# Performance work log

Hardware: AMD Instinct MI355X
Metric: run time of the kernel (lower is better)

The kernel has to match this reference:

```python
import jax, jax.numpy as jnp
import numpy as np

EPS = 1e-5
NEG = 0.1  # LeakyReLU slope


def _conv(x, w, stride=1, pad=0):
    return jax.lax.conv_general_dilated(
        x, w, (stride, stride), [(pad, pad), (pad, pad)],
        dimension_numbers=('NCHW', 'OIHW', 'NCHW'))


def _bn(x, p):
    # p: [4, C] stacked (gamma, beta, running_mean, running_var); eval-mode BN
    g, b, m, v = p[0], p[1], p[2], p[3]
    inv = g / jnp.sqrt(v + EPS)
    return x * inv[None, :, None, None] + (b - m * inv)[None, :, None, None]


def _lrelu(x):
    return jnp.where(x >= 0, x, NEG * x)


def _mdcn(x, w_off, b_off, w_dcn, b_dcn, G=2, K=3, pad=1):
    # ModulatedDeformConvPack (DCNv2): conv_offset -> (dy, dx, mask), then
    # modulated bilinear sampling + dense contraction with the conv weight.
    B, C, H, W = x.shape
    K2 = K * K
    off = _conv(x, w_off, 1, pad) + b_off[None, :, None, None]  # [B, 3*G*K2, H, W]
    dy, dx, ml = jnp.split(off, 3, axis=1)
    dy = dy.reshape(B, G, K2, H, W)
    dx = dx.reshape(B, G, K2, H, W)
    mask = jax.nn.sigmoid(ml).reshape(B, G, K2, H, W)
    kyv, kxv = np.meshgrid(np.arange(K), np.arange(K), indexing='ij')
    ky = jnp.asarray(kyv.reshape(K2), x.dtype)
    kx = jnp.asarray(kxv.reshape(K2), x.dtype)
    ii = jnp.arange(H, dtype=x.dtype)
    jj = jnp.arange(W, dtype=x.dtype)
    # sample coords: p0 + p_k + offset (stride 1, dilation 1)
    py = ii[None, None, None, :, None] - pad + ky[None, None, :, None, None] + dy
    px = jj[None, None, None, None, :] - pad + kx[None, None, :, None, None] + dx
    Cg = C // G
    # [B, G, H*W, Cg] layout so the bilinear gather indexes a small int tensor
    imgs = x.reshape(B, G, Cg, H, W).transpose(0, 1, 3, 4, 2).reshape(B, G, H * W, Cg)
    y0 = jnp.floor(py)
    x0 = jnp.floor(px)
    N = K2 * H * W
    wy = (py - y0).reshape(B, G, N, 1)
    wx = (px - x0).reshape(B, G, N, 1)

    def gather(yi, xi):
        valid = (yi >= 0) & (yi <= H - 1) & (xi >= 0) & (xi <= W - 1)
        yc = jnp.clip(yi, 0, H - 1).astype(jnp.int32)
        xc = jnp.clip(xi, 0, W - 1).astype(jnp.int32)
        idx = (yc * W + xc).reshape(B, G, N, 1)
        v = jnp.take_along_axis(imgs, idx, axis=2)  # [B, G, N, Cg]
        return v * valid.reshape(B, G, N, 1).astype(x.dtype)

    v00 = gather(y0, x0)
    v01 = gather(y0, x0 + 1)
    v10 = gather(y0 + 1, x0)
    v11 = gather(y0 + 1, x0 + 1)
    val = (v00 * (1 - wy) * (1 - wx) + v01 * (1 - wy) * wx
           + v10 * wy * (1 - wx) + v11 * wy * wx)
    val = (val * mask.reshape(B, G, N, 1)).reshape(B, G, K2, H, W, Cg)
    wr = w_dcn.reshape(w_dcn.shape[0], G, Cg, K2)
    out = jnp.einsum('bgkijc,ogck->boij', val, wr)
    return out + b_dcn[None, :, None, None]


def _forward(x, w_r1, bn_r1, w_r2, bn_r2, w_rs, bn_rs, w_off, b_off,
             w_dcn, b_dcn, bn1, w_c2, bn2, w_ds, bn_ds):
    # ResBlock(in=64, out=128, stride=2): conv3x3/s2-BN-LReLU-conv3x3-BN + 1x1/s2 shortcut
    h = _lrelu(_bn(_conv(x, w_r1, 2, 1), bn_r1))
    h = _bn(_conv(h, w_r2, 1, 1), bn_r2)
    sc = _bn(_conv(x, w_rs, 2, 0), bn_rs)
    h = _lrelu(h + sc)
    # modulated deformable conv 3x3, deformable_groups=2
    h = _lrelu(_bn(_mdcn(h, w_off, b_off, w_dcn, b_dcn), bn1))
    h = _lrelu(_bn(_conv(h, w_c2, 1, 0), bn2))
    # DeconBlock residual (downsample since in!=out, stride!=1)
    res = _bn(_conv(x, w_ds, 2, 0), bn_ds)
    return res + h


def setup_inputs() -> dict:
    key = jax.random.key(0)
    ks = jax.random.split(key, 16)
    f32 = jnp.float32

    def n(k, shape, s):
        return jax.random.normal(k, shape, f32) * s

    def bnp(k, c):
        # gamma, beta, mean, var — var kept >= 0.1 for stability
        return jax.random.uniform(k, (4, c), f32, 0.1, 1.0)

    return {
        'x': n(ks[0], (4, 64, 192, 192), 1.0),
        'w_r1': n(ks[1], (128, 64, 3, 3), 0.04),
        'bn_r1': bnp(ks[2], 128),
        'w_r2': n(ks[3], (128, 128, 3, 3), 0.03),
        'bn_r2': bnp(ks[4], 128),
        'w_rs': n(ks[5], (128, 64, 1, 1), 0.12),
        'bn_rs': bnp(ks[6], 128),
        'w_off': n(ks[7], (54, 128, 3, 3), 0.01),  # small => offsets of a few px
        'b_off': n(ks[8], (54,), 0.1),
        'w_dcn': n(ks[9], (128, 128, 3, 3), 0.03),
        'b_dcn': n(ks[10], (128,), 0.1),
        'bn1': bnp(ks[11], 128),
        'w_c2': n(ks[12], (128, 128, 1, 1), 0.09),
        'bn2': bnp(ks[13], 128),
        'w_ds': n(ks[14], (128, 64, 1, 1), 0.12),
        'bn_ds': bnp(ks[15], 128),
    }


def reference(x, w_r1, bn_r1, w_r2, bn_r2, w_rs, bn_rs, w_off, b_off,
              w_dcn, b_dcn, bn1, w_c2, bn2, w_ds, bn_ds):
    return _forward(x, w_r1, bn_r1, w_r2, bn_r2, w_rs, bn_rs, w_off, b_off,
                    w_dcn, b_dcn, bn1, w_c2, bn2, w_ds, bn_ds)
```

## Files before the change

kernel.cpp:

```cpp
#include <hip/hip_runtime.h>
#include <hip/hip_bf16.h>
#include <cstdint>

#define EPS 1e-5f
#define NEG 0.1f

using bfrag = __attribute__((ext_vector_type(8))) short;
using f32x4 = __attribute__((ext_vector_type(4))) float;
typedef unsigned short ushort_t;

constexpr int B_  = 4,  CIN = 64, H0 = 192, W0 = 192;
constexpr int C_  = 128, H_ = 96, W_ = 96;
constexpr int HW_ = H_ * W_;
constexpr int HW0 = H0 * W0;
constexpr int XS  = 194;
constexpr int TS  = 98;
constexpr int VSTR = 1160;

__device__ __forceinline__ ushort_t f2bf(float f) {
  unsigned u = __builtin_bit_cast(unsigned, f);
  u += 0x7fffu + ((u >> 16) & 1u);
  return (ushort_t)(u >> 16);
}
__device__ __forceinline__ float loF(unsigned d) {
  return __builtin_bit_cast(float, d << 16);
}
__device__ __forceinline__ float hiF(unsigned d) {
  return __builtin_bit_cast(float, d & 0xFFFF0000u);
}
__device__ __forceinline__ bfrag loadB(const ushort_t* p) {
  return *(const bfrag*)p;
}

#define MFMA4(A0, A1, B0, B1, ACC)                                             \
  ACC[0][0] = __builtin_amdgcn_mfma_f32_16x16x32_bf16(A0, B0, ACC[0][0], 0, 0, 0); \
  ACC[0][1] = __builtin_amdgcn_mfma_f32_16x16x32_bf16(A0, B1, ACC[0][1], 0, 0, 0); \
  ACC[1][0] = __builtin_amdgcn_mfma_f32_16x16x32_bf16(A1, B0, ACC[1][0], 0, 0, 0); \
  ACC[1][1] = __builtin_amdgcn_mfma_f32_16x16x32_bf16(A1, B1, ACC[1][1], 0, 0, 0);

__global__ __launch_bounds__(256)
void k_prep(const float* __restrict__ w_r1, const float* __restrict__ w_r2,
            const float* __restrict__ w_off, const float* __restrict__ w_dcn,
            const float* __restrict__ w_rs, const float* __restrict__ w_c2,
            const float* __restrict__ w_ds,
            ushort_t* __restrict__ wp_r1, ushort_t* __restrict__ wp_r2,
            ushort_t* __restrict__ wp_off, ushort_t* __restrict__ wp_dcn,
            ushort_t* __restrict__ wp_rs, ushort_t* __restrict__ wp_c2,
            ushort_t* __restrict__ wp_ds,
            ushort_t* __restrict__ xclp, ushort_t* __restrict__ t1p,
            ushort_t* __restrict__ t3p) {
  int bi = blockIdx.x;
  int tid = (int)threadIdx.x;
  auto pack3w = [&](const float* w, ushort_t* wp, int O, int C, int Opad, int b0) {
    int idx = (bi - b0) * 256 + tid;
    int e = idx & 7;
    int lane = (idx >> 3) & 63;
    int fb = idx >> 9;
    int OBQ = Opad / 16;
    int obq = fb % OBQ, s = fb / OBQ;
    int lr = lane & 15, lq = lane >> 4;
    int o = obq * 16 + lr;
    int cq = s % (C / 32), tap = s / (C / 32);
    int c = cq * 32 + lq * 8 + e;
    wp[idx] = (o < O) ? f2bf(w[((size_t)o * C + c) * 9 + tap]) : (ushort_t)0;
  };
  auto pack1w = [&](const float* w, ushort_t* wp, int O, int C, int Opad, int b0) {
    int idx = (bi - b0) * 256 + tid;
    int e = idx & 7;
    int lane = (idx >> 3) & 63;
    int fb = idx >> 9;
    int OBQ = Opad / 16;
    int obq = fb % OBQ, s = fb / OBQ;
    int lr = lane & 15, lq = lane >> 4;
    int o = obq * 16 + lr;
    int c = s * 32 + lq * 8 + e;
    wp[idx] = (o < O) ? f2bf(w[(size_t)o * C + c]) : (ushort_t)0;
  };
  auto border = [&](ushort_t* buf, int N, int C, int b0) {
    int idx = (bi - b0) * 256 + tid;
    int per = 4 * N - 4;
    if (idx >= per * 4) return;
    int b = idx / per, e = idx - b * per;
    int r, s;
    if (e < N) { r = 0; s = e; }
    else if (e < 2 * N) { r = N - 1; s = e - N; }
    else if (e < 3 * N - 2) { r = e - 2 * N + 1; s = 0; }
    else { r = e - (3 * N - 2) + 1; s = N - 1; }
    uint4* p = (uint4*)(buf + ((size_t)(b * N + r) * N + s) * C);
#pragma unroll
    for (int t = 0; t < 16; ++t) { if (t < C / 8) p[t] = make_uint4(0, 0, 0, 0); }
  };
  if      (bi <  288) pack3w(w_r1,  wp_r1, 128,  64, 128, 0);
  else if (bi <  864) pack3w(w_r2,  wp_r2, 128, 128, 128, 288);
  else if (bi < 1152) pack3w(w_off, wp_off, 54, 128,  64, 864);
  else if (bi < 1728) pack3w(w_dcn, wp_dcn, 128, 128, 128, 1152);
  else if (bi < 1760) pack1w(w_rs,  wp_rs, 128,  64, 128, 1728);
  else if (bi < 1824) pack1w(w_c2,  wp_c2, 128, 128, 128, 1760);
  else if (bi < 1856) pack1w(w_ds,  wp_ds, 128,  64, 128, 1824);
  else if (bi < 1869) border(xclp, XS, 64, 1856);
  else if (bi < 1876) border(t1p, TS, 128, 1869);
  else                border(t3p, TS, 128, 1876);
}

__global__ __launch_bounds__(256)
void k_xcl(const float* __restrict__ x, ushort_t* __restrict__ xclp) {
  __shared__ float tile[64][65];
  int tx = threadIdx.x, ty = threadIdx.y;
  int cx = blockIdx.x, y = blockIdx.y, b = blockIdx.z;
  const float* src = x + (size_t)b * CIN * HW0 + (size_t)y * W0 + cx * 64;
#pragma unroll
  for (int r = 0; r < 16; ++r) {
    int ch = r * 4 + ty;
    tile[ch][tx] = src[(size_t)ch * HW0 + tx];
  }
  __syncthreads();
  ushort_t* dst = xclp + ((size_t)(b * XS + y + 1) * XS + cx * 64 + 1) * 64;
#pragma unroll
  for (int r = 0; r < 16; ++r) {
    int pp = r * 4 + ty;
    dst[(size_t)pp * 64 + tx] = f2bf(tile[tx][pp]);
  }
}

__global__ __launch_bounds__(256)
void k_conv1(const ushort_t* __restrict__ xclp, const ushort_t* __restrict__ wp,
             const float* __restrict__ bnp, ushort_t* __restrict__ t1p) {
  __shared__ ushort_t at[5 * 66 * 64];
  int tid = threadIdx.x, lane = tid & 63, wv = tid >> 6;
  int lr = lane & 15, lq = lane >> 4, ob = wv * 32;
  int j0 = blockIdx.x * 32, i0 = blockIdx.y * 2, b = blockIdx.z;
  for (int t = tid; t < 2640; t += 256) {
    int ky = t / 528, r = t - ky * 528;
    int p = r >> 3, c8 = r & 7;
    const char* src = (const char*)(xclp +
        ((size_t)(b * XS + 2 * i0 + ky) * XS + 2 * j0) * 64) + p * 128 + c8 * 16;
    int db = ((ky * 66 + p) * 128 + c8 * 16) ^ (((p >> 1) & 7) << 4);
    *(uint4*)((char*)at + db) = *(const uint4*)src;
  }
  __syncthreads();
  f32x4 acc[2][2][2] = {};
#pragma unroll
  for (int tap = 0; tap < 9; ++tap) {
    int ky = tap / 3, kx = tap - 3 * ky;
    int pxa = 2 * lr + kx, pxb = 2 * (16 + lr) + kx;
#pragma unroll
    for (int cq = 0; cq < 2; ++cq) {
      int s = tap * 2 + cq;
      bfrag b0 = loadB(wp + (size_t)(s * 8 + wv * 2) * 512 + lane * 8);
      bfrag b1 = loadB(wp + (size_t)(s * 8 + wv * 2 + 1) * 512 + lane * 8);
#pragma unroll
      for (int r = 0; r < 2; ++r) {
        int kr = 2 * r + ky;
        bfrag a0 = *(const bfrag*)((const char*)at +
            (((kr * 66 + pxa) * 128 + cq * 64 + lq * 16) ^ (((pxa >> 1) & 7) << 4)));
        bfrag a1 = *(const bfrag*)((const char*)at +
            (((kr * 66 + pxb) * 128 + cq * 64 + lq * 16) ^ (((pxb >> 1) & 7) << 4)));
        MFMA4(a0, a1, b0, b1, acc[r]);
      }
    }
  }
#pragma unroll
  for (int r = 0; r < 2; ++r) {
    ushort_t* dst = t1p + ((size_t)(b * TS + i0 + r + 1) * TS + j0 + 1) * 128;
#pragma unroll
    for (int nf = 0; nf < 2; ++nf) {
      int o = ob + nf * 16 + lr;
      float inv = bnp[o] * rsqrtf(bnp[384 + o] + EPS);
      float bb = bnp[128 + o] - bnp[256 + o] * inv;
#pragma unroll
      for (int mf = 0; mf < 2; ++mf)
#pragma unroll
        for (int jj = 0; jj < 4; ++jj) {
          int pix = mf * 16 + 4 * lq + jj;
          float v = acc[r][mf][nf][jj] * inv + bb;
          v = v >= 0.f ? v : NEG * v;
          dst[(size_t)pix * 128 + o] = f2bf(v);
        }
    }
  }
}

__global__ __launch_bounds__(256)
void k_conv2(const ushort_t* __restrict__ t1p, const ushort_t* __restrict__ xclp,
             const ushort_t* __restrict__ wp2, const ushort_t* __restrict__ wprs,
             const float* __restrict__ bn2p, const float* __restrict__ bnsp,
             ushort_t* __restrict__ t3p) {
  __shared__ ushort_t at[4 * 34 * 128];
  int tid = threadIdx.x, lane = tid & 63, wv = tid >> 6;
  int lr = lane & 15, lq = lane >> 4, ob = wv * 32;
  int j0 = blockIdx.x * 32, i0 = blockIdx.y * 2, b = blockIdx.z;
  for (int t = tid; t < 2176; t += 256) {
    int ky = t / 544, r = t - ky * 544;
    int p = r >> 4, c16 = r & 15;
    const char* src = (const char*)(t1p +
        ((size_t)(b * TS + i0 + ky) * TS + j0) * 128) + p * 256 + c16 * 16;
    int db = ((ky * 34 + p) * 256 + c16 * 16) ^ ((p & 7) << 4);
    *(uint4*)((char*)at + db) = *(const uint4*)src;
  }
  __syncthreads();
  f32x4 acc[2][2][2] = {};
  f32x4 acs[2][2][2] = {};
#pragma unroll
  for (int tap = 0; tap < 9; ++tap) {
    int ky = tap / 3, kx = tap - 3 * ky;
    int pxa = lr + kx, pxb = 16 + lr + kx;
#pragma unroll
    for (int cq = 0; cq < 4; ++cq) {
      int s = tap * 4 + cq;
      bfrag b0 = loadB(wp2 + (size_t)(s * 8 + wv * 2) * 512 + lane * 8);
      bfrag b1 = loadB(wp2 + (size_t)(s * 8 + wv * 2 + 1) * 512 + lane * 8);
#pragma unroll
      for (int r = 0; r < 2; ++r) {
        int kr = r + ky;
        bfrag a0 = *(const bfrag*)((const char*)at +
            (((kr * 34 + pxa) * 256 + cq * 64 + lq * 16) ^ ((pxa & 7) << 4)));
        bfrag a1 = *(const bfrag*)((const char*)at +
            (((kr * 34 + pxb) * 256 + cq * 64 + lq * 16) ^ ((pxb & 7) << 4)));
        MFMA4(a0, a1, b0, b1, acc[r]);
      }
    }
  }
#pragma unroll
  for (int r = 0; r < 2; ++r) {
    const ushort_t* rowp = xclp + (size_t)(b * XS + 2 * (i0 + r) + 1) * XS * 64;
    const ushort_t* pa = rowp + (size_t)(2 * (j0 + lr) + 1) * 64 + 8 * lq;
    const ushort_t* pb = rowp + (size_t)(2 * (j0 + 16 + lr) + 1) * 64 + 8 * lq;
#pragma unroll
    for (int sq = 0; sq < 2; ++sq) {
      bfrag a0 = loadB(pa + sq * 32);
      bfrag a1 = loadB(pb + sq * 32);
      bfrag b0 = loadB(wprs + (size_t)(sq * 8 + wv * 2) * 512 + lane * 8);
      bfrag b1 = loadB(wprs + (size_t)(sq * 8 + wv * 2 + 1) * 512 + lane * 8);
      MFMA4(a0, a1, b0, b1, acs[r]);
    }
  }
#pragma unroll
  for (int r = 0; r < 2; ++r) {
    ushort_t* dst = t3p + ((size_t)(b * TS + i0 + r + 1) * TS + j0 + 1) * 128;
#pragma unroll
    for (int nf = 0; nf < 2; ++nf) {
      int o = ob + nf * 16 + lr;
      float i2 = bn2p[o] * rsqrtf(bn2p[384 + o] + EPS);
      float b2 = bn2p[128 + o] - bn2p[256 + o] * i2;
      float is = bnsp[o] * rsqrtf(bnsp[384 + o] + EPS);
      float bs = bnsp[128 + o] - bnsp[256 + o] * is;
#pragma unroll
      for (int mf = 0; mf < 2; ++mf)
#pragma unroll
        for (int jj = 0; jj < 4; ++jj) {
          int pix = mf * 16 + 4 * lq + jj;
          float h = acc[r][mf][nf][jj] * i2 + b2 + acs[r][mf][nf][jj] * is + bs;
          h = h >= 0.f ? h : NEG * h;
          dst[(size_t)pix * 128 + o] = f2bf(h);
        }
    }
  }
}

__global__ __launch_bounds__(128)
void k_convoff(const ushort_t* __restrict__ t3p, const ushort_t* __restrict__ wp,
               const float* __restrict__ boff, float* __restrict__ offb) {
  __shared__ ushort_t at[3 * 34 * 128];
  int tid = threadIdx.x, lane = tid & 63, wv = tid >> 6;
  int lr = lane & 15, lq = lane >> 4, ob = wv * 32;
  int j0 = blockIdx.x * 32, i = blockIdx.y, b = blockIdx.z;
  for (int t = tid; t < 1632; t += 128) {
    int ky = t / 544, r = t - ky * 544;
    int p = r >> 4, c16 = r & 15;
    const char* src = (const char*)(t3p +
        ((size_t)(b * TS + i + ky) * TS + j0) * 128) + p * 256 + c16 * 16;
    int db = ((ky * 34 + p) * 256 + c16 * 16) ^ ((p & 7) << 4);
    *(uint4*)((char*)at + db) = *(const uint4*)src;
  }
  __syncthreads();
  f32x4 acc[2][2] = {};
#pragma unroll
  for (int tap = 0; tap < 9; ++tap) {
    int ky = tap / 3, kx = tap - 3 * ky;
    int pxa = lr + kx, pxb = 16 + lr + kx;
#pragma unroll
    for (int cq = 0; cq < 4; ++cq) {
      bfrag a0 = *(const bfrag*)((const char*)at +
          (((ky * 34 + pxa) * 256 + cq * 64 + lq * 16) ^ ((pxa & 7) << 4)));
      bfrag a1 = *(const bfrag*)((const char*)at +
          (((ky * 34 + pxb) * 256 + cq * 64 + lq * 16) ^ ((pxb & 7) << 4)));
      int s = tap * 4 + cq;
      bfrag b0 = loadB(wp + (size_t)(s * 4 + wv * 2) * 512 + lane * 8);
      bfrag b1 = loadB(wp + (size_t)(s * 4 + wv * 2 + 1) * 512 + lane * 8);
      MFMA4(a0, a1, b0, b1, acc);
    }
  }
  float* dst = offb + ((size_t)b * HW_ + (size_t)i * W_ + j0) * 64;
#pragma unroll
  for (int nf = 0; nf < 2; ++nf) {
    int o = ob + nf * 16 + lr;
    float bias = (o < 54) ? boff[o] : 0.f;
#pragma unroll
    for (int mf = 0; mf < 2; ++mf)
#pragma unroll
      for (int jj = 0; jj < 4; ++jj) {
        int pix = mf * 16 + 4 * lq + jj;
        float v = (o < 54) ? acc[mf][nf][jj] + bias : 0.f;
        dst[(size_t)pix * 64 + o] = v;
      }
  }
}

__global__ __launch_bounds__(512)
void k_dcn(const ushort_t* __restrict__ t3p, const float* __restrict__ offb,
           const ushort_t* __restrict__ wp, const float* __restrict__ bdcn,
           const float* __restrict__ bnp, ushort_t* __restrict__ t4cl) {
  __shared__ ushort_t val[32 * VSTR];
  int tid = threadIdx.x;
  int j0 = blockIdx.x * 32, i = blockIdx.y, b = blockIdx.z;
  int lane = tid & 63, wv = tid >> 6;
  int gq = tid >> 4;
  int c16 = tid & 15;
  int gl = (gq & 3) * 16;

  int my_b0 = 0, my_b1 = 0;
  unsigned my_w00 = 0, my_w10 = 0, my_w01 = 0, my_w11 = 0;
  if (c16 < 9) {
    int k = c16;
    int ky = k / 3, kx = k - 3 * ky;
    int j = j0 + gq;
    const float* ob_ = offb + ((size_t)b * HW_ + (size_t)i * W_ + j) * 64;
#pragma unroll
    for (int g = 0; g < 2; ++g) {
      int gk = g * 9 + k;
      float dy = ob_[gk];
      float dx = ob_[18 + gk];
      float ml = ob_[36 + gk];
      float mk = 1.f / (1.f + __expf(-ml));
      float py = (float)(i - 1 + ky) + dy;
      float px = (float)(j - 1 + kx) + dx;
      float fy = floorf(py), fx = floorf(px);
      float wy = py - fy, wx = px - fx;
      int y0 = (int)fy, x0 = (int)fx;
      bool yv0 = (unsigned)y0 < 96u, yv1 = (unsigned)(y0 + 1) < 96u;
      bool xv0 = (unsigned)x0 < 96u, xv1 = (unsigned)(x0 + 1) < 96u;
      float w00 = (yv0 && xv0) ? (1.f - wy) * (1.f - wx) * mk : 0.f;
      float w01 = (yv0 && xv1) ? (1.f - wy) * wx * mk : 0.f;
      float w10 = (yv1 && xv0) ? wy * (1.f - wx) * mk : 0.f;
      float w11 = (yv1 && xv1) ? wy * wx * mk : 0.f;
      int yb = min(max(y0, -1), 95), xb = min(max(x0, -1), 95);
      int bb = (((yb + 1) * TS + xb + 1) * 128 + g * 64) * 2;
      unsigned pw0 = (unsigned)f2bf(w00) | ((unsigned)f2bf(w01) << 16);
      unsigned pw1 = (unsigned)f2bf(w10) | ((unsigned)f2bf(w11) << 16);
      if (g == 0) { my_b0 = bb; my_w00 = pw0; my_w10 = pw1; }
      else        { my_b1 = bb; my_w01 = pw0; my_w11 = pw1; }
    }
  }

  const char* imgb = (const char*)(t3p + (size_t)b * TS * TS * 128) + c16 * 8;
  char* vrow = (char*)val + gq * (VSTR * 2) + c16 * 8;

#pragma unroll
  for (int g = 0; g < 2; ++g) {
#pragma unroll
    for (int k = 0; k < 9; ++k) {
      int gb = __shfl(g == 0 ? my_b0 : my_b1, gl + k, 64);
      unsigned w0 = (unsigned)__shfl((int)(g == 0 ? my_w00 : my_w01), gl + k, 64);
      unsigned w1 = (unsigned)__shfl((int)(g == 0 ? my_w10 : my_w11), gl + k, 64);
      const char* pA = imgb + gb;
      uint2 d00 = *(const uint2*)pA;
      uint2 d01 = *(const uint2*)(pA + 256);
      uint2 d10 = *(const uint2*)(pA + TS * 256);
      uint2 d11 = *(const uint2*)(pA + TS * 256 + 256);
      float w00 = loF(w0), w01 = hiF(w0);
      float w10 = loF(w1), w11 = hiF(w1);
      unsigned o2[2];
#pragma unroll
      for (int t = 0; t < 2; ++t) {
        unsigned e00 = ((const unsigned*)&d00)[t];
        unsigned e01 = ((const unsigned*)&d01)[t];
        unsigned e10 = ((const unsigned*)&d10)[t];
        unsigned e11 = ((const unsigned*)&d11)[t];
        float slo = loF(e00) * w00 + loF(e01) * w01 + loF(e10) * w10 + loF(e11) * w11;
        float shi = hiF(e00) * w00 + hiF(e01) * w01 + hiF(e10) * w10 + hiF(e11) * w11;
        unsigned u0 = __builtin_bit_cast(unsigned, slo) + 0x8000u;
        unsigned u1 = __builtin_bit_cast(unsigned, shi) + 0x8000u;
        o2[t] = __builtin_amdgcn_perm(u1, u0, 0x07060302u);
      }
      *(uint2*)(vrow + k * 256 + g * 128) = make_uint2(o2[0], o2[1]);
    }
  }
  __syncthreads();

  int lr = lane & 15, lq = lane >> 4, ob = wv * 16;
  f32x4 acc0 = {}, acc1 = {};
  for (int s = 0; s < 36; ++s) {
    bfrag a0 = *(const bfrag*)&val[lr * VSTR + 32 * s + 8 * lq];
    bfrag a1 = *(const bfrag*)&val[(16 + lr) * VSTR + 32 * s + 8 * lq];
    bfrag b0 = loadB(wp + (size_t)(s * 8 + wv) * 512 + lane * 8);
    acc0 = __builtin_amdgcn_mfma_f32_16x16x32_bf16(a0, b0, acc0, 0, 0, 0);
    acc1 = __builtin_amdgcn_mfma_f32_16x16x32_bf16(a1, b0, acc1, 0, 0, 0);
  }

  {
    ushort_t* dst = t4cl + ((size_t)(b * 96 + i) * 96 + j0) * 128;
    int o = ob + lr;
    float inv = bnp[o] * rsqrtf(bnp[384 + o] + EPS);
    float bb = bnp[128 + o] - bnp[256 + o] * inv;
    float bd = bdcn[o];
#pragma unroll
    for (int jj = 0; jj < 4; ++jj) {
      int p0 = 4 * lq + jj;
      float r0 = (acc0[jj] + bd) * inv + bb;
      r0 = r0 >= 0.f ? r0 : NEG * r0;
      dst[(size_t)p0 * 128 + o] = f2bf(r0);
      float r1 = (acc1[jj] + bd) * inv + bb;
      r1 = r1 >= 0.f ? r1 : NEG * r1;
      dst[(size_t)(16 + p0) * 128 + o] = f2bf(r1);
    }
  }
}

__global__ __launch_bounds__(256)
void k_final(const ushort_t* __restrict__ t4cl, const ushort_t* __restrict__ xclp,
             const ushort_t* __restrict__ wpc2, const ushort_t* __restrict__ wpds,
             const float* __restrict__ bn2p, const float* __restrict__ bndsp,
             float* __restrict__ outp) {
  __shared__ float ol[128 * 36];
  int tid = threadIdx.x, lane = tid & 63, wv = tid >> 6;
  int lr = lane & 15, lq = lane >> 4, ob = wv * 32;
  int j0 = blockIdx.x * 32, i = blockIdx.y, b = blockIdx.z;
  f32x4 acc[2][2] = {};
  f32x4 acs[2][2] = {};
  {
    const ushort_t* rowp = t4cl + ((size_t)(b * 96 + i) * 96 + j0) * 128;
#pragma unroll
    for (int s = 0; s < 4; ++s) {
      bfrag a0 = loadB(rowp + (size_t)lr * 128 + s * 32 + 8 * lq);
      bfrag a1 = loadB(rowp + (size_t)(16 + lr) * 128 + s * 32 + 8 * lq);
      bfrag b0 = loadB(wpc2 + (size_t)(s * 8 + wv * 2) * 512 + lane * 8);
      bfrag b1 = loadB(wpc2 + (size_t)(s * 8 + wv * 2 + 1) * 512 + lane * 8);
      MFMA4(a0, a1, b0, b1, acc);
    }
  }
  {
    const ushort_t* rowx = xclp + (size_t)(b * XS + 2 * i + 1) * XS * 64;
    const ushort_t* pa = rowx + (size_t)(2 * (j0 + lr) + 1) * 64 + 8 * lq;
    const ushort_t* pb = rowx + (size_t)(2 * (j0 + 16 + lr) + 1) * 64 + 8 * lq;
#pragma unroll
    for (int s = 0; s < 2; ++s) {
      bfrag a0 = loadB(pa + s * 32);
      bfrag a1 = loadB(pb + s * 32);
      bfrag b0 = loadB(wpds + (size_t)(s * 8 + wv * 2) * 512 + lane * 8);
      bfrag b1 = loadB(wpds + (size_t)(s * 8 + wv * 2 + 1) * 512 + lane * 8);
      MFMA4(a0, a1, b0, b1, acs);
    }
  }
#pragma unroll
  for (int nf = 0; nf < 2; ++nf) {
    int o = ob + nf * 16 + lr;
    float i2 = bn2p[o] * rsqrtf(bn2p[384 + o] + EPS);
    float b2 = bn2p[128 + o] - bn2p[256 + o] * i2;
    float id = bndsp[o] * rsqrtf(bndsp[384 + o] + EPS);
    float bd = bndsp[128 + o] - bndsp[256 + o] * id;
#pragma unroll
    for (int mf = 0; mf < 2; ++mf)
#pragma unroll
      for (int jj = 0; jj < 4; ++jj) {
        int pix = mf * 16 + 4 * lq + jj;
        float h = acc[mf][nf][jj] * i2 + b2;
        h = h >= 0.f ? h : NEG * h;
        float res = acs[mf][nf][jj] * id + bd;
        ol[o * 36 + pix] = res + h;
      }
  }
  __syncthreads();
#pragma unroll
  for (int r = 0; r < 4; ++r) {
    int idx = r * 256 + tid;
    int o = idx >> 3, p4 = idx & 7;
    f32x4 v = *(const f32x4*)&ol[o * 36 + p4 * 4];
    *(f32x4*)&outp[((size_t)(b * C_ + o) * H_ + i) * W_ + j0 + p4 * 4] = v;
  }
}

extern "C" void kernel_launch(void* const* d_in, const int* in_sizes, int n_in,
                              void* d_out, int out_size, void* d_ws, size_t ws_size,
                              hipStream_t stream) {
  const float* x     = (const float*)d_in[0];
  const float* w_r1  = (const float*)d_in[1];
  const float* bn_r1 = (const float*)d_in[2];
  const float* w_r2  = (const float*)d_in[3];
  const float* bn_r2 = (const float*)d_in[4];
  const float* w_rs  = (const float*)d_in[5];
  const float* bn_rs = (const float*)d_in[6];
  const float* w_off = (const float*)d_in[7];
  const float* b_off = (const float*)d_in[8];
  const float* w_dcn = (const float*)d_in[9];
  const float* b_dcn = (const float*)d_in[10];
  const float* bn1   = (const float*)d_in[11];
  const float* w_c2  = (const float*)d_in[12];
  const float* bn2   = (const float*)d_in[13];
  const float* w_ds  = (const float*)d_in[14];
  const float* bn_ds = (const float*)d_in[15];
  float* out = (float*)d_out;

  ushort_t* base  = (ushort_t*)d_ws;
  ushort_t* xclp  = base;
  ushort_t* t1p   = base + 9634816;
  ushort_t* t3p   = base + 14552064;
  ushort_t* wp_r1 = base + 19469312;
  ushort_t* wp_r2 = wp_r1 + 73728;
  ushort_t* wp_off= wp_r2 + 147456;
  ushort_t* wp_dcn= wp_off + 73728;
  ushort_t* wp_rs = wp_dcn + 147456;
  ushort_t* wp_c2 = wp_rs + 8192;
  ushort_t* wp_ds = wp_c2 + 16384;
  float*    offb  = (float*)t1p;
  ushort_t* t4cl  = t1p;

  k_prep<<<1883, 256, 0, stream>>>(w_r1, w_r2, w_off, w_dcn, w_rs, w_c2, w_ds,
                                   wp_r1, wp_r2, wp_off, wp_dcn, wp_rs, wp_c2,
                                   wp_ds, xclp, t1p, t3p);

  k_xcl    <<<dim3(3, 192, 4), dim3(64, 4), 0, stream>>>(x, xclp);
  k_conv1  <<<dim3(3, 48, 4), 256, 0, stream>>>(xclp, wp_r1, bn_r1, t1p);
  k_conv2  <<<dim3(3, 48, 4), 256, 0, stream>>>(t1p, xclp, wp_r2, wp_rs, bn_r2, bn_rs, t3p);
  k_convoff<<<dim3(3, 96, 4), 128, 0, stream>>>(t3p, wp_off, b_off, offb);
  k_dcn    <<<dim3(3, 96, 4), 512, 0, stream>>>(t3p, offb, wp_dcn, b_dcn, bn1, t4cl);
  k_final  <<<dim3(3, 96, 4), 256, 0, stream>>>(t4cl, xclp, wp_c2, wp_ds, bn2, bn_ds, out);
}
```

Before: 128.1 us.

## Fuse offset conv into DCN kernel and merge input transpose into prep

The separate offset-convolution kernel is folded into the deformable-conv kernel. Each block now covers 16 pixels instead of 32, computes the 54 offset channels with MFMA (K split across two wave halves and reduced through LDS), and keeps the offsets in LDS instead of writing them to global memory. The NCHW-to-channel-last bf16 transpose of x is also moved into k_prep as extra blocks, which removes one more launch. The cost is a smaller per-block pixel tile, so each block does less work and reloads DCN weights more often.

Result: no change. 127.0 us (-0.9%).

```diff
diff --git a/kernel.cpp b/kernel.cpp
--- a/kernel.cpp
+++ b/kernel.cpp
@@ -39,7 +39,8 @@
   ACC[1][1] = __builtin_amdgcn_mfma_f32_16x16x32_bf16(A1, B1, ACC[1][1], 0, 0, 0);
 
 __global__ __launch_bounds__(256)
-void k_prep(const float* __restrict__ w_r1, const float* __restrict__ w_r2,
+void k_prep(const float* __restrict__ x,
+            const float* __restrict__ w_r1, const float* __restrict__ w_r2,
             const float* __restrict__ w_off, const float* __restrict__ w_dcn,
             const float* __restrict__ w_rs, const float* __restrict__ w_c2,
             const float* __restrict__ w_ds,
@@ -49,6 +50,7 @@
             ushort_t* __restrict__ wp_ds,
             ushort_t* __restrict__ xclp, ushort_t* __restrict__ t1p,
             ushort_t* __restrict__ t3p) {
+  __shared__ float tile[64][65];
   int bi = blockIdx.x;
   int tid = (int)threadIdx.x;
   auto pack3w = [&](const float* w, ushort_t* wp, int O, int C, int Opad, int b0) {
@@ -99,26 +101,26 @@
   else if (bi < 1856) pack1w(w_ds,  wp_ds, 128,  64, 128, 1824);
   else if (bi < 1869) border(xclp, XS, 64, 1856);
   else if (bi < 1876) border(t1p, TS, 128, 1869);
-  else                border(t3p, TS, 128, 1876);
-}
-
-__global__ __launch_bounds__(256)
-void k_xcl(const float* __restrict__ x, ushort_t* __restrict__ xclp) {
-  __shared__ float tile[64][65];
-  int tx = threadIdx.x, ty = threadIdx.y;
-  int cx = blockIdx.x, y = blockIdx.y, b = blockIdx.z;
-  const float* src = x + (size_t)b * CIN * HW0 + (size_t)y * W0 + cx * 64;
-#pragma unroll
-  for (int r = 0; r < 16; ++r) {
-    int ch = r * 4 + ty;
-    tile[ch][tx] = src[(size_t)ch * HW0 + tx];
-  }
-  __syncthreads();
-  ushort_t* dst = xclp + ((size_t)(b * XS + y + 1) * XS + cx * 64 + 1) * 64;
-#pragma unroll
-  for (int r = 0; r < 16; ++r) {
-    int pp = r * 4 + ty;
-    dst[(size_t)pp * 64 + tx] = f2bf(tile[tx][pp]);
+  else if (bi < 1883) border(t3p, TS, 128, 1876);
+  else {
+    int bx = bi - 1883;
+    int cx = bx % 3;
+    int rem = bx / 3;
+    int y = rem % 192, b = rem / 192;
+    int tx = tid & 63, ty = tid >> 6;
+    const float* src = x + (size_t)b * CIN * HW0 + (size_t)y * W0 + cx * 64;
+#pragma unroll
+    for (int r = 0; r < 16; ++r) {
+      int ch = r * 4 + ty;
+      tile[ch][tx] = src[(size_t)ch * HW0 + tx];
+    }
+    __syncthreads();
+    ushort_t* dst = xclp + ((size_t)(b * XS + y + 1) * XS + cx * 64 + 1) * 64;
+#pragma unroll
+    for (int r = 0; r < 16; ++r) {
+      int pp = r * 4 + ty;
+      dst[(size_t)pp * 64 + tx] = f2bf(tile[tx][pp]);
+    }
   }
 }
 
@@ -257,144 +259,130 @@
   }
 }
 
-__global__ __launch_bounds__(128)
-void k_convoff(const ushort_t* __restrict__ t3p, const ushort_t* __restrict__ wp,
-               const float* __restrict__ boff, float* __restrict__ offb) {
-  __shared__ ushort_t at[3 * 34 * 128];
-  int tid = threadIdx.x, lane = tid & 63, wv = tid >> 6;
-  int lr = lane & 15, lq = lane >> 4, ob = wv * 32;
-  int j0 = blockIdx.x * 32, i = blockIdx.y, b = blockIdx.z;
-  for (int t = tid; t < 1632; t += 128) {
-    int ky = t / 544, r = t - ky * 544;
-    int p = r >> 4, c16 = r & 15;
-    const char* src = (const char*)(t3p +
-        ((size_t)(b * TS + i + ky) * TS + j0) * 128) + p * 256 + c16 * 16;
-    int db = ((ky * 34 + p) * 256 + c16 * 16) ^ ((p & 7) << 4);
-    *(uint4*)((char*)at + db) = *(const uint4*)src;
-  }
-  __syncthreads();
-  f32x4 acc[2][2] = {};
-#pragma unroll
-  for (int tap = 0; tap < 9; ++tap) {
-    int ky = tap / 3, kx = tap - 3 * ky;
-    int pxa = lr + kx, pxb = 16 + lr + kx;
-#pragma unroll
-    for (int cq = 0; cq < 4; ++cq) {
-      bfrag a0 = *(const bfrag*)((const char*)at +
-          (((ky * 34 + pxa) * 256 + cq * 64 + lq * 16) ^ ((pxa & 7) << 4)));
-      bfrag a1 = *(const bfrag*)((const char*)at +
-          (((ky * 34 + pxb) * 256 + cq * 64 + lq * 16) ^ ((pxb & 7) << 4)));
-      int s = tap * 4 + cq;
-      bfrag b0 = loadB(wp + (size_t)(s * 4 + wv * 2) * 512 + lane * 8);
-      bfrag b1 = loadB(wp + (size_t)(s * 4 + wv * 2 + 1) * 512 + lane * 8);
-      MFMA4(a0, a1, b0, b1, acc);
-    }
-  }
-  float* dst = offb + ((size_t)b * HW_ + (size_t)i * W_ + j0) * 64;
-#pragma unroll
-  for (int nf = 0; nf < 2; ++nf) {
-    int o = ob + nf * 16 + lr;
-    float bias = (o < 54) ? boff[o] : 0.f;
-#pragma unroll
-    for (int mf = 0; mf < 2; ++mf)
+__global__ __launch_bounds__(512)
+void k_dcn(const ushort_t* __restrict__ t3p, const ushort_t* __restrict__ wpo,
+           const float* __restrict__ boff, const ushort_t* __restrict__ wp,
+           const float* __restrict__ bdcn, const float* __restrict__ bnp,
+           ushort_t* __restrict__ t4cl) {
+  __shared__ ushort_t val[16 * VSTR];
+  __shared__ float offb_lds[16 * 64];
+  int tid = threadIdx.x;
+  int j0 = blockIdx.x * 16, i = blockIdx.y, b = blockIdx.z;
+  int lane = tid & 63, wv = tid >> 6;
+  int lr = lane & 15, lq = lane >> 4;
+
+  {
+    char* at = (char*)val;
+    for (int t = tid; t < 864; t += 512) {
+      int ky = t / 288, r = t - ky * 288;
+      int p = r >> 4, c16b = r & 15;
+      const char* src = (const char*)(t3p +
+          ((size_t)(b * TS + i + ky) * TS + j0 + p) * 128) + c16b * 16;
+      int db = ((ky * 18 + p) * 256 + c16b * 16) ^ ((p & 7) << 4);
+      *(uint4*)(at + db) = *(const uint4*)src;
+    }
+    __syncthreads();
+    int ot = wv & 3, kh = wv >> 2;
+    f32x4 pacc = {};
+#pragma unroll
+    for (int s9 = 0; s9 < 18; ++s9) {
+      int s = kh * 18 + s9;
+      int tap = s >> 2, cq = s & 3;
+      int ky = tap / 3, kx = tap - 3 * ky;
+      int px = lr + kx;
+      bfrag a0 = *(const bfrag*)(at +
+          (((ky * 18 + px) * 256 + cq * 64 + lq * 16) ^ ((px & 7) << 4)));
+      bfrag b0 = loadB(wpo + (size_t)(s * 4 + ot) * 512 + lane * 8);
+      pacc = __builtin_amdgcn_mfma_f32_16x16x32_bf16(a0, b0, pacc, 0, 0, 0);
+    }
+    float* red = (float*)((char*)val + 16384);
+    if (kh == 1) {
+      *(f32x4*)(red + ot * 256 + lane * 4) = pacc;
+    }
+    __syncthreads();
+    if (kh == 0) {
+      f32x4 v = *(const f32x4*)(red + ot * 256 + lane * 4);
+      pacc += v;
+      int o = ot * 16 + lr;
+      float bias = (o < 54) ? boff[o] : 0.f;
 #pragma unroll
       for (int jj = 0; jj < 4; ++jj) {
-        int pix = mf * 16 + 4 * lq + jj;
-        float v = (o < 54) ? acc[mf][nf][jj] + bias : 0.f;
-        dst[(size_t)pix * 64 + o] = v;
+        int px = 4 * lq + jj;
+        offb_lds[px * 64 + o] = pacc[jj] + bias;
       }
-  }
-}
-
-__global__ __launch_bounds__(512)
-void k_dcn(const ushort_t* __restrict__ t3p, const float* __restrict__ offb,
-           const ushort_t* __restrict__ wp, const float* __restrict__ bdcn,
-           const float* __restrict__ bnp, ushort_t* __restrict__ t4cl) {
-  __shared__ ushort_t val[32 * VSTR];
-  int tid = threadIdx.x;
-  int j0 = blockIdx.x * 32, i = blockIdx.y, b = blockIdx.z;
-  int lane = tid & 63, wv = tid >> 6;
+    }
+    __syncthreads();
+  }
+
   int gq = tid >> 4;
   int c16 = tid & 15;
+  int pix = gq >> 1, g = gq & 1;
   int gl = (gq & 3) * 16;
-
-  int my_b0 = 0, my_b1 = 0;
-  unsigned my_w00 = 0, my_w10 = 0, my_w01 = 0, my_w11 = 0;
+  int my_b = 0; unsigned my_w0 = 0, my_w1 = 0;
   if (c16 < 9) {
-    int k = c16;
+    int k = c16, gk = g * 9 + k;
     int ky = k / 3, kx = k - 3 * ky;
-    int j = j0 + gq;
-    const float* ob_ = offb + ((size_t)b * HW_ + (size_t)i * W_ + j) * 64;
-#pragma unroll
-    for (int g = 0; g < 2; ++g) {
-      int gk = g * 9 + k;
-      float dy = ob_[gk];
-      float dx = ob_[18 + gk];
-      float ml = ob_[36 + gk];
-      float mk = 1.f / (1.f + __expf(-ml));
-      float py = (float)(i - 1 + ky) + dy;
-      float px = (float)(j - 1 + kx) + dx;
-      float fy = floorf(py), fx = floorf(px);
-      float wy = py - fy, wx = px - fx;
-      int y0 = (int)fy, x0 = (int)fx;
-      bool yv0 = (unsigned)y0 < 96u, yv1 = (unsigned)(y0 + 1) < 96u;
-      bool xv0 = (unsigned)x0 < 96u, xv1 = (unsigned)(x0 + 1) < 96u;
-      float w00 = (yv0 && xv0) ? (1.f - wy) * (1.f - wx) * mk : 0.f;
-      float w01 = (yv0 && xv1) ? (1.f - wy) * wx * mk : 0.f;
-      float w10 = (yv1 && xv0) ? wy * (1.f - wx) * mk : 0.f;
-      float w11 = (yv1 && xv1) ? wy * wx * mk : 0.f;
-      int yb = min(max(y0, -1), 95), xb = min(max(x0, -1), 95);
-      int bb = (((yb + 1) * TS + xb + 1) * 128 + g * 64) * 2;
-      unsigned pw0 = (unsigned)f2bf(w00) | ((unsigned)f2bf(w01) << 16);
-      unsigned pw1 = (unsigned)f2bf(w10) | ((unsigned)f2bf(w11) << 16);
-      if (g == 0) { my_b0 = bb; my_w00 = pw0; my_w10 = pw1; }
-      else        { my_b1 = bb; my_w01 = pw0; my_w11 = pw1; }
-    }
-  }
+    int j = j0 + pix;
+    const float* ob_ = offb_lds + pix * 64;
+    float dy = ob_[gk];
+    float dx = ob_[18 + gk];
+    float ml = ob_[36 + gk];
+    float mk = 1.f / (1.f + __expf(-ml));
+    float py = (float)(i - 1 + ky) + dy;
+    float px = (float)(j - 1 + kx) + dx;
+    float fy = floorf(py), fx = floorf(px);
+    float wy = py - fy, wx = px - fx;
+    int y0 = (int)fy, x0 = (int)fx;
+    bool yv0 = (unsigned)y0 < 96u, yv1 = (unsigned)(y0 + 1) < 96u;
+    bool xv0 = (unsigned)x0 < 96u, xv1 = (unsigned)(x0 + 1) < 96u;
+    float w00 = (yv0 && xv0) ? (1.f - wy) * (1.f - wx) * mk : 0.f;
+    float w01 = (yv0 && xv1) ? (1.f - wy) * wx * mk : 0.f;
+    float w10 = (yv1 && xv0) ? wy * (1.f - wx) * mk : 0.f;
+    float w11 = (yv1 && xv1) ? wy * wx * mk : 0.f;
+    int yb = min(max(y0, -1), 95), xb = min(max(x0, -1), 95);
+    my_b = (((yb + 1) * TS + xb + 1) * 128 + g * 64) * 2;
+    my_w0 = (unsigned)f2bf(w00) | ((unsigned)f2bf(w01) << 16);
+    my_w1 = (unsigned)f2bf(w10) | ((unsigned)f2bf(w11) << 16);
+  }
+  __syncthreads();
 
   const char* imgb = (const char*)(t3p + (size_t)b * TS * TS * 128) + c16 * 8;
-  char* vrow = (char*)val + gq * (VSTR * 2) + c16 * 8;
-
-#pragma unroll
-  for (int g = 0; g < 2; ++g) {
-#pragma unroll
-    for (int k = 0; k < 9; ++k) {
-      int gb = __shfl(g == 0 ? my_b0 : my_b1, gl + k, 64);
-      unsigned w0 = (unsigned)__shfl((int)(g == 0 ? my_w00 : my_w01), gl + k, 64);
-      unsigned w1 = (unsigned)__shfl((int)(g == 0 ? my_w10 : my_w11), gl + k, 64);
-      const char* pA = imgb + gb;
-      uint2 d00 = *(const uint2*)pA;
-      uint2 d01 = *(const uint2*)(pA + 256);
-      uint2 d10 = *(const uint2*)(pA + TS * 256);
-      uint2 d11 = *(const uint2*)(pA + TS * 256 + 256);
-      float w00 = loF(w0), w01 = hiF(w0);
-      float w10 = loF(w1), w11 = hiF(w1);
-      unsigned o2[2];
-#pragma unroll
-      for (int t = 0; t < 2; ++t) {
-        unsigned e00 = ((const unsigned*)&d00)[t];
-        unsigned e01 = ((const unsigned*)&d01)[t];
-        unsigned e10 = ((const unsigned*)&d10)[t];
-        unsigned e11 = ((const unsigned*)&d11)[t];
-        float slo = loF(e00) * w00 + loF(e01) * w01 + loF(e10) * w10 + loF(e11) * w11;
-        float shi = hiF(e00) * w00 + hiF(e01) * w01 + hiF(e10) * w10 + hiF(e11) * w11;
-        unsigned u0 = __builtin_bit_cast(unsigned, slo) + 0x8000u;
-        unsigned u1 = __builtin_bit_cast(unsigned, shi) + 0x8000u;
-        o2[t] = __builtin_amdgcn_perm(u1, u0, 0x07060302u);
-      }
-      *(uint2*)(vrow + k * 256 + g * 128) = make_uint2(o2[0], o2[1]);
-    }
+  char* vrow = (char*)val + pix * (VSTR * 2) + g * 128 + c16 * 8;
+#pragma unroll
+  for (int k = 0; k < 9; ++k) {
+    int gb = __shfl(my_b, gl + k, 64);
+    unsigned w0 = (unsigned)__shfl((int)my_w0, gl + k, 64);
+    unsigned w1 = (unsigned)__shfl((int)my_w1, gl + k, 64);
+    const char* pA = imgb + gb;
+    uint2 d00 = *(const uint2*)pA;
+    uint2 d01 = *(const uint2*)(pA + 256);
+    uint2 d10 = *(const uint2*)(pA + TS * 256);
+    uint2 d11 = *(const uint2*)(pA + TS * 256 + 256);
+    float w00 = loF(w0), w01 = hiF(w0);
+    float w10 = loF(w1), w11 = hiF(w1);
+    unsigned o2[2];
+#pragma unroll
+    for (int t = 0; t < 2; ++t) {
+      unsigned e00 = ((const unsigned*)&d00)[t];
+      unsigned e01 = ((const unsigned*)&d01)[t];
+      unsigned e10 = ((const unsigned*)&d10)[t];
+      unsigned e11 = ((const unsigned*)&d11)[t];
+      float slo = loF(e00) * w00 + loF(e01) * w01 + loF(e10) * w10 + loF(e11) * w11;
+      float shi = hiF(e00) * w00 + hiF(e01) * w01 + hiF(e10) * w10 + hiF(e11) * w11;
+      unsigned u0 = __builtin_bit_cast(unsigned, slo) + 0x8000u;
+      unsigned u1 = __builtin_bit_cast(unsigned, shi) + 0x8000u;
+      o2[t] = __builtin_amdgcn_perm(u1, u0, 0x07060302u);
+    }
+    *(uint2*)(vrow + k * 256) = make_uint2(o2[0], o2[1]);
   }
   __syncthreads();
 
-  int lr = lane & 15, lq = lane >> 4, ob = wv * 16;
-  f32x4 acc0 = {}, acc1 = {};
+  int ob = wv * 16;
+  f32x4 acc = {};
   for (int s = 0; s < 36; ++s) {
     bfrag a0 = *(const bfrag*)&val[lr * VSTR + 32 * s + 8 * lq];
-    bfrag a1 = *(const bfrag*)&val[(16 + lr) * VSTR + 32 * s + 8 * lq];
     bfrag b0 = loadB(wp + (size_t)(s * 8 + wv) * 512 + lane * 8);
-    acc0 = __builtin_amdgcn_mfma_f32_16x16x32_bf16(a0, b0, acc0, 0, 0, 0);
-    acc1 = __builtin_amdgcn_mfma_f32_16x16x32_bf16(a1, b0, acc1, 0, 0, 0);
+    acc = __builtin_amdgcn_mfma_f32_16x16x32_bf16(a0, b0, acc, 0, 0, 0);
   }
 
   {
@@ -405,13 +393,10 @@
     float bd = bdcn[o];
 #pragma unroll
     for (int jj = 0; jj < 4; ++jj) {
-      int p0 = 4 * lq + jj;
-      float r0 = (acc0[jj] + bd) * inv + bb;
-      r0 = r0 >= 0.f ? r0 : NEG * r0;
-      dst[(size_t)p0 * 128 + o] = f2bf(r0);
-      float r1 = (acc1[jj] + bd) * inv + bb;
-      r1 = r1 >= 0.f ? r1 : NEG * r1;
-      dst[(size_t)(16 + p0) * 128 + o] = f2bf(r1);
+      int pixw = 4 * lq + jj;
+      float r = (acc[jj] + bd) * inv + bb;
+      r = r >= 0.f ? r : NEG * r;
+      dst[(size_t)pixw * 128 + o] = f2bf(r);
     }
   }
 }
@@ -511,17 +496,14 @@
   ushort_t* wp_rs = wp_dcn + 147456;
   ushort_t* wp_c2 = wp_rs + 8192;
   ushort_t* wp_ds = wp_c2 + 16384;
-  float*    offb  = (float*)t1p;
   ushort_t* t4cl  = t1p;
 
-  k_prep<<<1883, 256, 0, stream>>>(w_r1, w_r2, w_off, w_dcn, w_rs, w_c2, w_ds,
-                                   wp_r1, wp_r2, wp_off, wp_dcn, wp_rs, wp_c2,
-                                   wp_ds, xclp, t1p, t3p);
-
-  k_xcl    <<<dim3(3, 192, 4), dim3(64, 4), 0, stream>>>(x, xclp);
-  k_conv1  <<<dim3(3, 48, 4), 256, 0, stream>>>(xclp, wp_r1, bn_r1, t1p);
-  k_conv2  <<<dim3(3, 48, 4), 256, 0, stream>>>(t1p, xclp, wp_r2, wp_rs, bn_r2, bn_rs, t3p);
-  k_convoff<<<dim3(3, 96, 4), 128, 0, stream>>>(t3p, wp_off, b_off, offb);
-  k_dcn    <<<dim3(3, 96, 4), 512, 0, stream>>>(t3p, offb, wp_dcn, b_dcn, bn1, t4cl);
-  k_final  <<<dim3(3, 96, 4), 256, 0, stream>>>(t4cl, xclp, wp_c2, wp_ds, bn2, bn_ds, out);
-}
+  k_prep<<<4187, 256, 0, stream>>>(x, w_r1, w_r2, w_off, w_dcn, w_rs, w_c2,
+                                   w_ds, wp_r1, wp_r2, wp_off, wp_dcn, wp_rs,
+                                   wp_c2, wp_ds, xclp, t1p, t3p);
+
+  k_conv1<<<dim3(3, 48, 4), 256, 0, stream>>>(xclp, wp_r1, bn_r1, t1p);
+  k_conv2<<<dim3(3, 48, 4), 256, 0, stream>>>(t1p, xclp, wp_r2, wp_rs, bn_r2, bn_rs, t3p);
+  k_dcn  <<<dim3(6, 96, 4), 512, 0, stream>>>(t3p, wp_off, b_off, wp_dcn, b_dcn, bn1, t4cl);
+  k_final<<<dim3(3, 96, 4), 256, 0, stream>>>(t4cl, xclp, wp_c2, wp_ds, bn2, bn_ds, out);
+}
```
